# Kernel optimization log

Hardware: AMD Instinct MI355X
Metric: run time of the kernel (lower is better)

Reference implementation:

```python
import jax, jax.numpy as jnp
import numpy as np

NUM_HEADS = 16
KEY_SIZE = 64
HEAD_SIZE = 64


def setup_inputs() -> dict:
    key = jax.random.key(0)
    ks = jax.random.split(key, 8)
    B, S, D = 2, 2048, 1024
    s = 1.0 / np.sqrt(D)
    return {
        "q": jax.random.normal(ks[0], (B, S, D), jnp.float32),
        "k": jax.random.normal(ks[1], (B, S, D), jnp.float32),
        "v": jax.random.normal(ks[2], (B, S, D), jnp.float32),
        "v_mask": jax.random.randint(ks[3], (B, S), 0, 2, jnp.int32),
        "Wq": jax.random.normal(ks[4], (D, NUM_HEADS * KEY_SIZE), jnp.float32) * s,
        "Wk": jax.random.normal(ks[5], (D, NUM_HEADS * KEY_SIZE), jnp.float32) * s,
        "Wv": jax.random.normal(ks[6], (D, NUM_HEADS * HEAD_SIZE), jnp.float32) * s,
    }


def reference(q, k, v, v_mask, Wq, Wk, Wv):
    B, Sq, _ = q.shape
    Sk = k.shape[1]
    # projections + split heads: [B, S, H, d]
    qw = (q @ Wq).reshape(B, Sq, NUM_HEADS, KEY_SIZE)
    kw = (k @ Wk).reshape(B, Sk, NUM_HEADS, KEY_SIZE)
    vw = (v @ Wv).reshape(B, Sk, NUM_HEADS, HEAD_SIZE)
    # scores [B, H, Sq, Sk]
    a = jnp.einsum('bqhd,bkhd->bhqk', qw, kw) / np.sqrt(KEY_SIZE).astype(np.float32)
    # additive mask over key axis: x*m - (1-m)*1e12
    m = v_mask.astype(a.dtype)[:, None, None, :]
    a = a * m - (1.0 - m) * 1e12
    a = jax.nn.softmax(a, axis=-1)
    # output [B, Sq, H*head_size]
    o = jnp.einsum('bhqk,bkhd->bqhd', a, vw)
    return o.reshape(B, Sq, NUM_HEADS * HEAD_SIZE)
```

## Files before the change

kernel.cpp:

```cpp
#include <hip/hip_runtime.h>
#include <hip/hip_bf16.h>


#define SEQ 2048
#define DIM 1024
#define NPROJ 1024

typedef __bf16 bf16x8 __attribute__((ext_vector_type(8)));
typedef float floatx4 __attribute__((ext_vector_type(4)));
typedef float floatx16 __attribute__((ext_vector_type(16)));

__device__ inline unsigned short f2bf_bits(float x) {
  __hip_bfloat16 h = __float2bfloat16(x);
  return __builtin_bit_cast(unsigned short, h);
}

__device__ __forceinline__ void gload_lds16(const void* g, void* l) {
  __builtin_amdgcn_global_load_lds((const __attribute__((address_space(1))) void*)g,
                                   (__attribute__((address_space(3))) void*)l, 16, 0, 0);
}

__global__ __launch_bounds__(256) void transpose_w(
    const float* __restrict__ Wq, const float* __restrict__ Wk, const float* __restrict__ Wv,
    unsigned short* __restrict__ WqT, unsigned short* __restrict__ WkT, unsigned short* __restrict__ WvT)
{
  const float* W = blockIdx.z == 0 ? Wq : (blockIdx.z == 1 ? Wk : Wv);
  unsigned short* WT = blockIdx.z == 0 ? WqT : (blockIdx.z == 1 ? WkT : WvT);
  const float sc = (blockIdx.z == 0) ? 0.1803368801f : 1.0f;
  __shared__ float tile[64][65];
  const int k0 = blockIdx.x * 64;
  const int n0 = blockIdx.y * 64;
  const int t = threadIdx.x;
  #pragma unroll
  for (int it = 0; it < 4; ++it) {
    int idx = t + (it << 8);
    int r = idx >> 4, c4 = (idx & 15) << 2;
    float4 v = *reinterpret_cast<const float4*>(&W[(k0 + r) * DIM + n0 + c4]);
    tile[r][c4 + 0] = v.x; tile[r][c4 + 1] = v.y;
    tile[r][c4 + 2] = v.z; tile[r][c4 + 3] = v.w;
  }
  __syncthreads();
  #pragma unroll
  for (int it = 0; it < 4; ++it) {
    int idx = t + (it << 8);
    int r = idx >> 4, c4 = (idx & 15) << 2;
    ushort4 o;
    o.x = f2bf_bits(tile[c4 + 0][r] * sc);
    o.y = f2bf_bits(tile[c4 + 1][r] * sc);
    o.z = f2bf_bits(tile[c4 + 2][r] * sc);
    o.w = f2bf_bits(tile[c4 + 3][r] * sc);
    *reinterpret_cast<ushort4*>(&WT[(n0 + r) * DIM + k0 + c4]) = o;
  }
}

__global__ __launch_bounds__(256, 4) void proj_gemm(
    const float* __restrict__ xq, const float* __restrict__ xk, const float* __restrict__ xv,
    const unsigned short* __restrict__ WqT, const unsigned short* __restrict__ WkT,
    const unsigned short* __restrict__ WvT,
    unsigned short* __restrict__ qw, unsigned short* __restrict__ kw, unsigned short* __restrict__ vw)
{
  const float* X = blockIdx.z == 0 ? xq : (blockIdx.z == 1 ? xk : xv);
  const unsigned short* WT = blockIdx.z == 0 ? WqT : (blockIdx.z == 1 ? WkT : WvT);
  unsigned short* Y = blockIdx.z == 0 ? qw : (blockIdx.z == 1 ? kw : vw);

  __shared__ unsigned short Al[2][128 * 32];
  __shared__ unsigned short Bl[2][128 * 32];

  const int m0 = blockIdx.x * 128, n0 = blockIdx.y * 128;
  const int t = threadIdx.x;
  const int lane = t & 63;
  const int wid = t >> 6;
  const int wm = (wid >> 1) << 6, wn = (wid & 1) << 6;
  const int qd = lane >> 4, ln = lane & 15;

  float4 ra[2], rb[2];

  auto loadA = [&](int ks) {
    #pragma unroll
    for (int i = 0; i < 2; ++i) {
      int p = t + (i << 8);
      int r = p >> 2, c = p & 3;
      int f = (r + (r >> 2)) & 3;
      const float* ga = X + (size_t)(m0 + r) * 1024 + ks * 32 + ((c ^ f) << 3);
      ra[i] = *reinterpret_cast<const float4*>(ga);
      rb[i] = *reinterpret_cast<const float4*>(ga + 4);
    }
  };
  auto writeA = [&](int bi) {
    #pragma unroll
    for (int i = 0; i < 2; ++i) {
      int p = t + (i << 8);
      struct alignas(16) { unsigned short u[8]; } pk;
      pk.u[0] = f2bf_bits(ra[i].x); pk.u[1] = f2bf_bits(ra[i].y);
      pk.u[2] = f2bf_bits(ra[i].z); pk.u[3] = f2bf_bits(ra[i].w);
      pk.u[4] = f2bf_bits(rb[i].x); pk.u[5] = f2bf_bits(rb[i].y);
      pk.u[6] = f2bf_bits(rb[i].z); pk.u[7] = f2bf_bits(rb[i].w);
      *reinterpret_cast<int4*>((char*)&Al[bi][0] + p * 16) =
          *reinterpret_cast<const int4*>(pk.u);
    }
  };
  auto loadB = [&](int ks, int bi) {
    #pragma unroll
    for (int i = 0; i < 2; ++i) {
      int p = t + (i << 8);
      int r = p >> 2, c = p & 3;
      int f = (r + (r >> 2)) & 3;
      gload_lds16((const char*)WT + (size_t)(n0 + r) * 2048 + (ks << 6) + ((c ^ f) << 4),
                  (char*)&Bl[bi][0] + p * 16);
    }
  };

  floatx4 acc[4][4] = {};
  loadB(0, 0);
  loadA(0);
  writeA(0);
  loadA(1);

  for (int ks = 0; ks < 32; ++ks) {
    __syncthreads();
    const int bi = ks & 1;
    if (ks + 1 < 32) {
      loadB(ks + 1, bi ^ 1);
      writeA(bi ^ 1);
    }
    if (ks + 2 < 32) loadA(ks + 2);

    bf16x8 af[4], bfr[4];
    #pragma unroll
    for (int mb = 0; mb < 4; ++mb) {
      int m = wm + mb * 16 + ln;
      int fm = (m + (m >> 2)) & 3;
      af[mb] = *reinterpret_cast<const bf16x8*>(&Al[bi][m * 32 + ((qd ^ fm) << 3)]);
    }
    #pragma unroll
    for (int nb = 0; nb < 4; ++nb) {
      int n = wn + nb * 16 + ln;
      int fn = (n + (n >> 2)) & 3;
      bfr[nb] = *reinterpret_cast<const bf16x8*>(&Bl[bi][n * 32 + ((qd ^ fn) << 3)]);
    }
    #pragma unroll
    for (int mb = 0; mb < 4; ++mb)
      #pragma unroll
      for (int nb = 0; nb < 4; ++nb)
        acc[mb][nb] = __builtin_amdgcn_mfma_f32_16x16x32_bf16(af[mb], bfr[nb], acc[mb][nb], 0, 0, 0);
  }
  #pragma unroll
  for (int mb = 0; mb < 4; ++mb)
    #pragma unroll
    for (int nb = 0; nb < 4; ++nb)
      #pragma unroll
      for (int i = 0; i < 4; ++i) {
        int m = m0 + wm + mb * 16 + qd * 4 + i;
        int n = n0 + wn + nb * 16 + ln;
        Y[(size_t)m * NPROJ + n] = f2bf_bits(acc[mb][nb][i]);
      }
}

__global__ __launch_bounds__(256) void transpose_v(
    const unsigned short* __restrict__ vw, const int* __restrict__ vmask,
    unsigned short* __restrict__ vt, unsigned short* __restrict__ mb)
{
  if (blockIdx.y == 0 && blockIdx.x < 16) {
    int i = blockIdx.x * 256 + threadIdx.x;
    mb[i] = vmask[i] ? 0x3F80 : 0;
  }
  __shared__ unsigned short tile[64 * 64];
  const int t = threadIdx.x;
  const int s0 = blockIdx.x * 64;
  const int bh = blockIdx.y;
  const int b = bh >> 4, h = bh & 15;
  #pragma unroll
  for (int it = 0; it < 2; ++it) {
    int p = t + (it << 8);
    int s = p >> 3, c = p & 7;
    int cp = (c + (s >> 3) + (s & 7)) & 7;
    int4 d = *reinterpret_cast<const int4*>(&vw[(size_t)(b * SEQ + s0 + s) * NPROJ + h * 64 + c * 8]);
    if (vmask[b * SEQ + s0 + s] == 0) { d.x = 0; d.y = 0; d.z = 0; d.w = 0; }
    *reinterpret_cast<int4*>(&tile[s * 64 + cp * 8]) = d;
  }
  __syncthreads();
  #pragma unroll
  for (int it = 0; it < 2; ++it) {
    int d = (t >> 3) + (it << 5), sc = t & 7;
    struct { alignas(16) unsigned short u[8]; } o;
    #pragma unroll
    for (int j = 0; j < 8; ++j) {
      int s = sc * 8 + j;
      int cp = ((d >> 3) + (s >> 3) + (s & 7)) & 7;
      o.u[j] = tile[s * 64 + cp * 8 + (d & 7)];
    }
    *reinterpret_cast<int4*>(&vt[(size_t)(bh * 64 + d) * SEQ + s0 + sc * 8]) =
        *reinterpret_cast<const int4*>(o.u);
  }
}

__global__ __launch_bounds__(512, 2) void attn_fwd(
    const unsigned short* __restrict__ qw, const unsigned short* __restrict__ kw,
    const unsigned short* __restrict__ vt, const unsigned short* __restrict__ mb,
    float* __restrict__ out)
{
  extern __shared__ char smem[];
  unsigned short* Kl = (unsigned short*)smem;
  unsigned short* Vl = (unsigned short*)(smem + 16384);
  unsigned short* Ml = (unsigned short*)(smem + 32768);

  const int t = threadIdx.x, lane = t & 63, wid = t >> 6;
  const int l5 = lane & 31, hi = lane >> 5;
  const int qh = wid >> 1, kh = wid & 1;
  const int bh = blockIdx.x;
  const int q0 = blockIdx.y * 256;
  const int b = bh >> 4, h = bh & 15;
  const int base = b * SEQ;

  auto stage = [&](int kt, int bi) {
    const int k0 = kt << 6;
    int rb = wid * 8;
    int r = rb + (lane >> 3);
    int rsrc = (r & ~12) | ((r & 4) << 1) | ((r & 8) >> 1);
    int sw = ((lane & 7) ^ (r & 7)) << 4;
    gload_lds16((const char*)kw + ((size_t)((base + k0 + rsrc) * NPROJ + h * 64) << 1) + sw,
                (char*)&Kl[bi * 4096] + rb * 128);
    gload_lds16((const char*)vt + ((size_t)((bh * 64 + r) * SEQ + k0) << 1) + sw,
                (char*)&Vl[bi * 4096] + rb * 128);
    if (wid == 7 && lane < 8)
      gload_lds16((const char*)mb + ((size_t)(base + k0 + lane * 8) << 1), (char*)&Ml[bi * 64]);
  };

  bf16x8 qfa[4], qfb[4];
  {
    const unsigned short* qpa =
        qw + (size_t)(base + q0 + qh * 64 + l5) * NPROJ + h * 64 + hi * 8;
    const unsigned short* qpb = qpa + (size_t)32 * NPROJ;
    #pragma unroll
    for (int kk = 0; kk < 4; ++kk) {
      qfa[kk] = *reinterpret_cast<const bf16x8*>(qpa + kk * 16);
      qfb[kk] = *reinterpret_cast<const bf16x8*>(qpb + kk * 16);
    }
  }

  floatx16 oa0a = {}, oa1a = {}, laa = {};
  floatx16 oa0b = {}, oa1b = {}, lab = {};
  stage(0, 0);

  #pragma unroll 2
  for (int kt = 0; kt < SEQ / 64; ++kt) {
    __syncthreads();
    if (kt + 1 < SEQ / 64) stage(kt + 1, (kt + 1) & 1);
    const int bi = kt & 1;

    floatx16 sa = {}, sb = {};
    __builtin_amdgcn_s_setprio(1);
    #pragma unroll
    for (int kk = 0; kk < 4; ++kk) {
      int ph = ((kk * 2 + hi) ^ (l5 & 7)) << 3;
      bf16x8 kf = *reinterpret_cast<const bf16x8*>(&Kl[bi * 4096 + (kh * 32 + l5) * 64 + ph]);
      sa = __builtin_amdgcn_mfma_f32_32x32x16_bf16(kf, qfa[kk], sa, 0, 0, 0);
      sb = __builtin_amdgcn_mfma_f32_32x32x16_bf16(kf, qfb[kk], sb, 0, 0, 0);
    }
    __builtin_amdgcn_s_setprio(0);

    float pea[16], peb[16];
    #pragma unroll
    for (int r = 0; r < 16; ++r) {
      pea[r] = __builtin_amdgcn_exp2f(sa[r]);
      peb[r] = __builtin_amdgcn_exp2f(sb[r]);
    }

    #pragma unroll
    for (int kk = 0; kk < 2; ++kk) {
      struct alignas(16) { unsigned short u[8]; } pka, pkb;
      #pragma unroll
      for (int j = 0; j < 8; ++j) {
        pka.u[j] = f2bf_bits(pea[8 * kk + j]);
        pkb.u[j] = f2bf_bits(peb[8 * kk + j]);
      }
      bf16x8 paa = __builtin_bit_cast(bf16x8, pka);
      bf16x8 pab = __builtin_bit_cast(bf16x8, pkb);
      int ch = ((4 * kh + 2 * kk + hi) ^ (l5 & 7)) << 3;
      bf16x8 v0 = *reinterpret_cast<const bf16x8*>(&Vl[bi * 4096 + l5 * 64 + ch]);
      bf16x8 v1 = *reinterpret_cast<const bf16x8*>(&Vl[bi * 4096 + (32 + l5) * 64 + ch]);
      bf16x8 mf = *reinterpret_cast<const bf16x8*>(&Ml[bi * 64 + kh * 32 + kk * 16 + hi * 8]);
      __builtin_amdgcn_s_setprio(1);
      oa0a = __builtin_amdgcn_mfma_f32_32x32x16_bf16(paa, v0, oa0a, 0, 0, 0);
      oa1a = __builtin_amdgcn_mfma_f32_32x32x16_bf16(paa, v1, oa1a, 0, 0, 0);
      laa  = __builtin_amdgcn_mfma_f32_32x32x16_bf16(paa, mf, laa, 0, 0, 0);
      oa0b = __builtin_amdgcn_mfma_f32_32x32x16_bf16(pab, v0, oa0b, 0, 0, 0);
      oa1b = __builtin_amdgcn_mfma_f32_32x32x16_bf16(pab, v1, oa1b, 0, 0, 0);
      lab  = __builtin_amdgcn_mfma_f32_32x32x16_bf16(pab, mf, lab, 0, 0, 0);
      __builtin_amdgcn_s_setprio(0);
    }
  }

  __syncthreads();
  float* Mg = (float*)smem;
  if (kh == 1) {
    #pragma unroll
    for (int r = 0; r < 16; ++r) {
      int m = (r & 3) + ((r >> 2) << 3) + (hi << 2);
      int rowa = qh * 64 + m, rowb = qh * 64 + 32 + m;
      Mg[rowa * 66 + l5] = oa0a[r];
      Mg[rowa * 66 + 32 + l5] = oa1a[r];
      Mg[rowb * 66 + l5] = oa0b[r];
      Mg[rowb * 66 + 32 + l5] = oa1b[r];
      if (l5 == 0) { Mg[rowa * 66 + 64] = laa[r]; Mg[rowb * 66 + 64] = lab[r]; }
    }
  }
  __syncthreads();
  if (kh == 0) {
    #pragma unroll
    for (int r = 0; r < 16; ++r) {
      int m = (r & 3) + ((r >> 2) << 3) + (hi << 2);
      int rowa = qh * 64 + m, rowb = qh * 64 + 32 + m;
      float o0a = oa0a[r] + Mg[rowa * 66 + l5];
      float o1a = oa1a[r] + Mg[rowa * 66 + 32 + l5];
      float inva = 1.0f / (laa[r] + Mg[rowa * 66 + 64]);
      size_t oa_ = (size_t)(base + q0 + rowa) * NPROJ + h * 64;
      out[oa_ + l5] = o0a * inva;
      out[oa_ + 32 + l5] = o1a * inva;
      float o0b = oa0b[r] + Mg[rowb * 66 + l5];
      float o1b = oa1b[r] + Mg[rowb * 66 + 32 + l5];
      float invb = 1.0f / (lab[r] + Mg[rowb * 66 + 64]);
      size_t ob_ = (size_t)(base + q0 + rowb) * NPROJ + h * 64;
      out[ob_ + l5] = o0b * invb;
      out[ob_ + 32 + l5] = o1b * invb;
    }
  }
}

extern "C" void kernel_launch(void* const* d_in, const int* in_sizes, int n_in,
                              void* d_out, int out_size, void* d_ws, size_t ws_size,
                              hipStream_t stream) {
  const float* q  = (const float*)d_in[0];
  const float* k  = (const float*)d_in[1];
  const float* v  = (const float*)d_in[2];
  const int* vm   = (const int*)d_in[3];
  const float* Wq = (const float*)d_in[4];
  const float* Wk = (const float*)d_in[5];
  const float* Wv = (const float*)d_in[6];
  float* out = (float*)d_out;

  unsigned short* ws = (unsigned short*)d_ws;
  unsigned short* WqT = ws + ((size_t)0 << 20);
  unsigned short* WkT = ws + ((size_t)1 << 20);
  unsigned short* WvT = ws + ((size_t)2 << 20);
  unsigned short* qw  = ws + ((size_t)3 << 20);
  unsigned short* kw  = ws + ((size_t)7 << 20);
  unsigned short* vw  = ws + ((size_t)11 << 20);
  unsigned short* vt  = ws + ((size_t)15 << 20);
  unsigned short* mbv = WqT;

  transpose_w<<<dim3(16, 16, 3), 256, 0, stream>>>(Wq, Wk, Wv, WqT, WkT, WvT);
  proj_gemm<<<dim3(32, 8, 3), 256, 0, stream>>>(q, k, v, WqT, WkT, WvT, qw, kw, vw);
  transpose_v<<<dim3(32, 32), 256, 0, stream>>>(vw, vm, vt, mbv);
  attn_fwd<<<dim3(32, 8), 512, 67584, stream>>>(qw, kw, vt, mbv, out);
}
```

Measured before the change: 92.73 us.

## Fuse V transpose and masking into projection GEMM epilogue

The V projection GEMM epilogue now writes its output directly in the transposed per-head layout, zeroing masked key rows, which removes the separate transpose_v kernel and its read and write of the V intermediate. The mask-to-bf16 conversion moves into the weight transpose kernel, and its buffer moves to a dedicated workspace slot. This saves one launch and a round trip through global memory. The cost is that the transposed epilogue issues 8-byte strided stores across rows of length SEQ, which coalesce worse than the old row-major stores.

```diff
diff --git a/kernel.cpp b/kernel.cpp
--- a/kernel.cpp
+++ b/kernel.cpp
@@ -22,8 +22,14 @@
 
 __global__ __launch_bounds__(256) void transpose_w(
     const float* __restrict__ Wq, const float* __restrict__ Wk, const float* __restrict__ Wv,
-    unsigned short* __restrict__ WqT, unsigned short* __restrict__ WkT, unsigned short* __restrict__ WvT)
+    const int* __restrict__ vmask,
+    unsigned short* __restrict__ WqT, unsigned short* __restrict__ WkT, unsigned short* __restrict__ WvT,
+    unsigned short* __restrict__ mb)
 {
+  if (blockIdx.z == 1 && blockIdx.y == 0 && blockIdx.x < 16) {
+    int i = blockIdx.x * 256 + threadIdx.x;
+    mb[i] = vmask[i] ? 0x3F80 : 0;
+  }
   const float* W = blockIdx.z == 0 ? Wq : (blockIdx.z == 1 ? Wk : Wv);
   unsigned short* WT = blockIdx.z == 0 ? WqT : (blockIdx.z == 1 ? WkT : WvT);
   const float sc = (blockIdx.z == 0) ? 0.1803368801f : 1.0f;
@@ -56,15 +62,15 @@
 __global__ __launch_bounds__(256, 4) void proj_gemm(
     const float* __restrict__ xq, const float* __restrict__ xk, const float* __restrict__ xv,
     const unsigned short* __restrict__ WqT, const unsigned short* __restrict__ WkT,
-    const unsigned short* __restrict__ WvT,
-    unsigned short* __restrict__ qw, unsigned short* __restrict__ kw, unsigned short* __restrict__ vw)
+    const unsigned short* __restrict__ WvT, const int* __restrict__ vmask,
+    unsigned short* __restrict__ qw, unsigned short* __restrict__ kw, unsigned short* __restrict__ vt)
 {
   const float* X = blockIdx.z == 0 ? xq : (blockIdx.z == 1 ? xk : xv);
   const unsigned short* WT = blockIdx.z == 0 ? WqT : (blockIdx.z == 1 ? WkT : WvT);
-  unsigned short* Y = blockIdx.z == 0 ? qw : (blockIdx.z == 1 ? kw : vw);
 
   __shared__ unsigned short Al[2][128 * 32];
   __shared__ unsigned short Bl[2][128 * 32];
+  __shared__ int vml[128];
 
   const int m0 = blockIdx.x * 128, n0 = blockIdx.y * 128;
   const int t = threadIdx.x;
@@ -72,6 +78,8 @@
   const int wid = t >> 6;
   const int wm = (wid >> 1) << 6, wn = (wid & 1) << 6;
   const int qd = lane >> 4, ln = lane & 15;
+
+  if (blockIdx.z == 2 && t < 128) vml[t] = vmask[m0 + t];
 
   float4 ra[2], rb[2];
 
@@ -144,53 +152,38 @@
       for (int nb = 0; nb < 4; ++nb)
         acc[mb][nb] = __builtin_amdgcn_mfma_f32_16x16x32_bf16(af[mb], bfr[nb], acc[mb][nb], 0, 0, 0);
   }
-  #pragma unroll
-  for (int mb = 0; mb < 4; ++mb)
-    #pragma unroll
-    for (int nb = 0; nb < 4; ++nb)
+
+  if (blockIdx.z != 2) {
+    unsigned short* Y = blockIdx.z == 0 ? qw : kw;
+    #pragma unroll
+    for (int mb = 0; mb < 4; ++mb)
       #pragma unroll
-      for (int i = 0; i < 4; ++i) {
-        int m = m0 + wm + mb * 16 + qd * 4 + i;
+      for (int nb = 0; nb < 4; ++nb)
+        #pragma unroll
+        for (int i = 0; i < 4; ++i) {
+          int m = m0 + wm + mb * 16 + qd * 4 + i;
+          int n = n0 + wn + nb * 16 + ln;
+          Y[(size_t)m * NPROJ + n] = f2bf_bits(acc[mb][nb][i]);
+        }
+  } else {
+    const int b = m0 >> 11;
+    const int sbase = (m0 & 2047) + wm + qd * 4;
+    #pragma unroll
+    for (int mb = 0; mb < 4; ++mb) {
+      int mloc = wm + mb * 16 + qd * 4;
+      int s = sbase + mb * 16;
+      #pragma unroll
+      for (int nb = 0; nb < 4; ++nb) {
         int n = n0 + wn + nb * 16 + ln;
-        Y[(size_t)m * NPROJ + n] = f2bf_bits(acc[mb][nb][i]);
+        size_t row = (size_t)(b * 16 + (n >> 6)) * 64 + (n & 63);
+        ushort4 o;
+        o.x = vml[mloc + 0] ? f2bf_bits(acc[mb][nb][0]) : (unsigned short)0;
+        o.y = vml[mloc + 1] ? f2bf_bits(acc[mb][nb][1]) : (unsigned short)0;
+        o.z = vml[mloc + 2] ? f2bf_bits(acc[mb][nb][2]) : (unsigned short)0;
+        o.w = vml[mloc + 3] ? f2bf_bits(acc[mb][nb][3]) : (unsigned short)0;
+        *reinterpret_cast<ushort4*>(&vt[row * SEQ + s]) = o;
       }
-}
-
-__global__ __launch_bounds__(256) void transpose_v(
-    const unsigned short* __restrict__ vw, const int* __restrict__ vmask,
-    unsigned short* __restrict__ vt, unsigned short* __restrict__ mb)
-{
-  if (blockIdx.y == 0 && blockIdx.x < 16) {
-    int i = blockIdx.x * 256 + threadIdx.x;
-    mb[i] = vmask[i] ? 0x3F80 : 0;
-  }
-  __shared__ unsigned short tile[64 * 64];
-  const int t = threadIdx.x;
-  const int s0 = blockIdx.x * 64;
-  const int bh = blockIdx.y;
-  const int b = bh >> 4, h = bh & 15;
-  #pragma unroll
-  for (int it = 0; it < 2; ++it) {
-    int p = t + (it << 8);
-    int s = p >> 3, c = p & 7;
-    int cp = (c + (s >> 3) + (s & 7)) & 7;
-    int4 d = *reinterpret_cast<const int4*>(&vw[(size_t)(b * SEQ + s0 + s) * NPROJ + h * 64 + c * 8]);
-    if (vmask[b * SEQ + s0 + s] == 0) { d.x = 0; d.y = 0; d.z = 0; d.w = 0; }
-    *reinterpret_cast<int4*>(&tile[s * 64 + cp * 8]) = d;
-  }
-  __syncthreads();
-  #pragma unroll
-  for (int it = 0; it < 2; ++it) {
-    int d = (t >> 3) + (it << 5), sc = t & 7;
-    struct { alignas(16) unsigned short u[8]; } o;
-    #pragma unroll
-    for (int j = 0; j < 8; ++j) {
-      int s = sc * 8 + j;
-      int cp = ((d >> 3) + (s >> 3) + (s & 7)) & 7;
-      o.u[j] = tile[s * 64 + cp * 8 + (d & 7)];
-    }
-    *reinterpret_cast<int4*>(&vt[(size_t)(bh * 64 + d) * SEQ + s0 + sc * 8]) =
-        *reinterpret_cast<const int4*>(o.u);
+    }
   }
 }
 
@@ -345,12 +338,10 @@
   unsigned short* WvT = ws + ((size_t)2 << 20);
   unsigned short* qw  = ws + ((size_t)3 << 20);
   unsigned short* kw  = ws + ((size_t)7 << 20);
-  unsigned short* vw  = ws + ((size_t)11 << 20);
+  unsigned short* mbv = ws + ((size_t)11 << 20);
   unsigned short* vt  = ws + ((size_t)15 << 20);
-  unsigned short* mbv = WqT;
-
-  transpose_w<<<dim3(16, 16, 3), 256, 0, stream>>>(Wq, Wk, Wv, WqT, WkT, WvT);
-  proj_gemm<<<dim3(32, 8, 3), 256, 0, stream>>>(q, k, v, WqT, WkT, WvT, qw, kw, vw);
-  transpose_v<<<dim3(32, 32), 256, 0, stream>>>(vw, vm, vt, mbv);
+
+  transpose_w<<<dim3(16, 16, 3), 256, 0, stream>>>(Wq, Wk, Wv, vm, WqT, WkT, WvT, mbv);
+  proj_gemm<<<dim3(32, 8, 3), 256, 0, stream>>>(q, k, v, WqT, WkT, WvT, vm, qw, kw, vt);
   attn_fwd<<<dim3(32, 8), 512, 67584, stream>>>(qw, kw, vt, mbv, out);
 }
```

New measurement: 91.25 us (median of 7 runs). No clear change (-1.6%).
